# Optimization experiments

Measured on AMD Instinct MI355X. Metric: run time of the kernel, lower is better.

Reference implementation:

```python
import jax, jax.numpy as jnp
import numpy as np

DIM = 1024
DEPTH = 2
HEADS = 16
MLP = 4096
HEAD_DIM = DIM // HEADS
EPS = 1e-5


def layernorm(x, w, b):
    mu = jnp.mean(x, axis=-1, keepdims=True)
    var = jnp.mean(jnp.square(x - mu), axis=-1, keepdims=True)
    return (x - mu) * jax.lax.rsqrt(var + EPS) * w + b


def setup_inputs() -> dict:
    key = jax.random.key(0)
    ks = jax.random.split(key, 16)
    s = 0.02
    x = jax.random.normal(ks[0], (2, 2048, DIM), dtype=jnp.float32)
    inp = {
        "x": x,
        "ln1_w": jnp.ones((DEPTH, DIM), jnp.float32),
        "ln1_b": jnp.zeros((DEPTH, DIM), jnp.float32),
        "qkv_w": jax.random.normal(ks[1], (DEPTH, DIM, 3 * DIM), jnp.float32) * s,
        "qkv_b": jnp.zeros((DEPTH, 3 * DIM), jnp.float32),
        "in_w": jax.random.normal(ks[2], (DEPTH, DIM, 3 * DIM), jnp.float32) * s,
        "in_b": jnp.zeros((DEPTH, 3 * DIM), jnp.float32),
        "out_w": jax.random.normal(ks[3], (DEPTH, DIM, DIM), jnp.float32) * s,
        "out_b": jnp.zeros((DEPTH, DIM), jnp.float32),
        "ln2_w": jnp.ones((DEPTH, DIM), jnp.float32),
        "ln2_b": jnp.zeros((DEPTH, DIM), jnp.float32),
        "w1": jax.random.normal(ks[4], (DEPTH, DIM, MLP), jnp.float32) * s,
        "b1": jnp.zeros((DEPTH, MLP), jnp.float32),
        "w2": jax.random.normal(ks[5], (DEPTH, MLP, DIM), jnp.float32) * s,
        "b2": jnp.zeros((DEPTH, DIM), jnp.float32),
    }
    return inp


def _forward(x, ln1_w, ln1_b, qkv_w, qkv_b, in_w, in_b, out_w, out_b,
             ln2_w, ln2_b, w1, b1, w2, b2):
    B, S, D = x.shape
    scale = 1.0 / jnp.sqrt(jnp.float32(HEAD_DIM))
    for i in range(DEPTH):
        # --- Attention block (pre-norm) ---
        h = layernorm(x, ln1_w[i], ln1_b[i])
        qkv = h @ qkv_w[i] + qkv_b[i]                      # [B,S,3D]
        q, k, v = jnp.split(qkv, 3, axis=-1)
        # nn.MultiheadAttention's own in_proj on top of to_qkv
        qp = q @ in_w[i][:, :D] + in_b[i][:D]
        kp = k @ in_w[i][:, D:2 * D] + in_b[i][D:2 * D]
        vp = v @ in_w[i][:, 2 * D:] + in_b[i][2 * D:]
        qp = qp.reshape(B, S, HEADS, HEAD_DIM)
        kp = kp.reshape(B, S, HEADS, HEAD_DIM)
        vp = vp.reshape(B, S, HEADS, HEAD_DIM)
        scores = jnp.einsum("bqhd,bkhd->bhqk", qp, kp) * scale
        attn = jax.nn.softmax(scores, axis=-1)
        o = jnp.einsum("bhqk,bkhd->bqhd", attn, vp).reshape(B, S, D)
        o = o @ out_w[i] + out_b[i]
        x = o + x
        # --- FFN block (pre-norm) ---
        h = layernorm(x, ln2_w[i], ln2_b[i])
        h = jax.nn.gelu(h @ w1[i] + b1[i], approximate=False)
        h = h @ w2[i] + b2[i]
        x = h + x
    return x


def reference(x, ln1_w, ln1_b, qkv_w, qkv_b, in_w, in_b, out_w, out_b,
              ln2_w, ln2_b, w1, b1, w2, b2):
    return _forward(x, ln1_w, ln1_b, qkv_w, qkv_b, in_w, in_b, out_w, out_b,
                    ln2_w, ln2_b, w1, b1, w2, b2)
```

## Files before the change

kernel.cpp:

```cpp
#include <hip/hip_runtime.h>
#include <math.h>

#define D_MODEL 1024
#define NHEADS 16
#define HEAD_DIM 64
#define SEQ 2048
#define BATCH 2
#define TOK (BATCH*SEQ)
#define MLP_DIM 4096

#define F_BIAS  1
#define F_GELU  2

typedef __attribute__((ext_vector_type(8))) __bf16 bf16x8;
typedef __attribute__((ext_vector_type(16))) __bf16 bf16x16;
typedef __attribute__((ext_vector_type(4))) __bf16 bf16x4;
typedef __attribute__((ext_vector_type(4))) float f32x4;

__device__ __forceinline__ void gload16(const void* g, void* l) {
    __builtin_amdgcn_global_load_lds(
        (const __attribute__((address_space(1))) void*)g,
        (__attribute__((address_space(3))) void*)l, 16, 0, 0);
}

__global__ __launch_bounds__(256)
void conv_kernel(const float* __restrict__ in, __bf16* __restrict__ out, int n8)
{
    const int idx = blockIdx.x * 256 + threadIdx.x;
    if (idx >= n8) return;
    const float4 a = *(const float4*)(in + idx * 8);
    const float4 b = *(const float4*)(in + idx * 8 + 4);
    bf16x8 o;
    o[0] = (__bf16)a.x; o[1] = (__bf16)a.y; o[2] = (__bf16)a.z; o[3] = (__bf16)a.w;
    o[4] = (__bf16)b.x; o[5] = (__bf16)b.y; o[6] = (__bf16)b.z; o[7] = (__bf16)b.w;
    *(bf16x8*)(out + idx * 8) = o;
}

__global__ __launch_bounds__(256)
void tconv64_kernel(const float* __restrict__ in, __bf16* __restrict__ out, int R, int C)
{
    __shared__ __bf16 tile[64][72];
    const int bx = blockIdx.x;
    const int by = blockIdx.y;
    const int t = threadIdx.x;
    const int rl = t >> 4, cl = (t & 15) * 4;
    #pragma unroll
    for (int rr = 0; rr < 4; ++rr) {
        const float4 v = *(const float4*)&in[(size_t)(by * 64 + rr * 16 + rl) * C + bx * 64 + cl];
        tile[rr * 16 + rl][cl + 0] = (__bf16)v.x;
        tile[rr * 16 + rl][cl + 1] = (__bf16)v.y;
        tile[rr * 16 + rl][cl + 2] = (__bf16)v.z;
        tile[rr * 16 + rl][cl + 3] = (__bf16)v.w;
    }
    __syncthreads();
    const int oc = t >> 2, rs = (t & 3) * 16;
    bf16x16 y;
    #pragma unroll
    for (int k = 0; k < 16; ++k) y[k] = tile[rs + k][oc];
    *(bf16x16*)&out[(size_t)(bx * 64 + oc) * R + by * 64 + rs] = y;
}

__global__ __launch_bounds__(256)
void bcomb_kernel(const float* __restrict__ qkv_b, const float* __restrict__ in_w,
                  const float* __restrict__ in_b, float* __restrict__ bc)
{
    const int t = blockIdx.x * 256 + threadIdx.x;
    const int p = t >> 10, n = t & 1023;
    float s = in_b[t];
    #pragma unroll 16
    for (int k = 0; k < D_MODEL; ++k)
        s = fmaf(qkv_b[p * D_MODEL + k], in_w[(size_t)k * 3 * D_MODEL + p * D_MODEL + n], s);
    bc[t] = s;
}

__global__ __launch_bounds__(256)
void tv_kernel(const __bf16* __restrict__ v, __bf16* __restrict__ vt)
{
    __shared__ __bf16 t[64][72];
    const int bh = blockIdx.y, b = bh >> 4, h = bh & 15;
    const int s0 = blockIdx.x * 64;
    const int r = threadIdx.x >> 3;
    const int c = (threadIdx.x & 7) * 8;
    #pragma unroll
    for (int rr = 0; rr < 64; rr += 32) {
        bf16x8 x = *(const bf16x8*)&v[(size_t)(b * SEQ + s0 + r + rr) * D_MODEL + h * 64 + c];
        #pragma unroll
        for (int k = 0; k < 8; ++k) t[r + rr][c + k] = x[k];
    }
    __syncthreads();
    #pragma unroll
    for (int rr = 0; rr < 64; rr += 32) {
        bf16x8 y;
        #pragma unroll
        for (int k = 0; k < 8; ++k) y[k] = t[c + k][r + rr];
        *(bf16x8*)&vt[((size_t)bh * 64 + r + rr) * SEQ + s0 + c] = y;
    }
}

__device__ __forceinline__ void ln_body(float4 v, const float* w, const float* b,
                                        __bf16* out, int row, int t)
{
    float s  = v.x + v.y + v.z + v.w;
    float ss = v.x*v.x + v.y*v.y + v.z*v.z + v.w*v.w;
    #pragma unroll
    for (int off = 32; off > 0; off >>= 1) {
        s  += __shfl_down(s, off);
        ss += __shfl_down(ss, off);
    }
    __shared__ float red[8];
    const int wid = t >> 6, lane = t & 63;
    if (lane == 0) { red[wid] = s; red[4 + wid] = ss; }
    __syncthreads();
    const float st  = red[0] + red[1] + red[2] + red[3];
    const float sst = red[4] + red[5] + red[6] + red[7];
    const float mu  = st * (1.0f / D_MODEL);
    const float var = sst * (1.0f / D_MODEL) - mu * mu;
    const float rs  = rsqrtf(var + 1e-5f);
    const float4 wv = *(const float4*)(w + t * 4);
    const float4 bv = *(const float4*)(b + t * 4);
    bf16x4 o;
    o[0] = (__bf16)((v.x - mu) * rs * wv.x + bv.x);
    o[1] = (__bf16)((v.y - mu) * rs * wv.y + bv.y);
    o[2] = (__bf16)((v.z - mu) * rs * wv.z + bv.z);
    o[3] = (__bf16)((v.w - mu) * rs * wv.w + bv.w);
    *(bf16x4*)(out + (size_t)row * D_MODEL + t * 4) = o;
}

__global__ __launch_bounds__(256)
void ln_kernel(const float* __restrict__ x, const float* __restrict__ w,
               const float* __restrict__ b, __bf16* __restrict__ out)
{
    const int row = blockIdx.x, t = threadIdx.x;
    float4 v = *(const float4*)(x + (size_t)row * D_MODEL + t * 4);
    ln_body(v, w, b, out, row, t);
}

__global__ __launch_bounds__(256)
void ln_add_kernel(float* __restrict__ x, const float* __restrict__ p0,
                   const float* __restrict__ p1, const float* __restrict__ w,
                   const float* __restrict__ b, __bf16* __restrict__ out)
{
    const int row = blockIdx.x, t = threadIdx.x;
    const size_t idx = (size_t)row * D_MODEL + t * 4;
    float4 v  = *(const float4*)(x + idx);
    float4 a0 = *(const float4*)(p0 + idx);
    float4 a1 = *(const float4*)(p1 + idx);
    v.x += a0.x + a1.x; v.y += a0.y + a1.y;
    v.z += a0.z + a1.z; v.w += a0.w + a1.w;
    *(float4*)(x + idx) = v;
    ln_body(v, w, b, out, row, t);
}

__global__ __launch_bounds__(256)
void add2_kernel(float* __restrict__ x, const float* __restrict__ p0,
                 const float* __restrict__ p1)
{
    const size_t idx = ((size_t)blockIdx.x * 256 + threadIdx.x) * 4;
    float4 v  = *(const float4*)(x + idx);
    float4 a0 = *(const float4*)(p0 + idx);
    float4 a1 = *(const float4*)(p1 + idx);
    v.x += a0.x + a1.x; v.y += a0.y + a1.y;
    v.z += a0.z + a1.z; v.w += a0.w + a1.w;
    *(float4*)(x + idx) = v;
}

__device__ __forceinline__ void mgemm_acc(
    const __bf16* __restrict__ A, int lda,
    const __bf16* __restrict__ Bt, int ldb, int K,
    __bf16* As, __bf16* Bs, f32x4 (&acc)[4][4])
{
    const int tid  = threadIdx.x;
    const int lane = tid & 63;
    const int w    = tid >> 6;
    const int wm   = w >> 1, wn = w & 1;
    const int bm = blockIdx.y, bn = blockIdx.x;

    const int s1 = 256 + tid;
    const int kc0 = tid >> 7, r0 = tid & 127;
    const int kc1 = s1  >> 7, r1 = s1 & 127;

    const __bf16* a0p = A  + (size_t)(bm * 128 + r0) * lda + kc0 * 8;
    const __bf16* a1p = A  + (size_t)(bm * 128 + r1) * lda + kc1 * 8;
    const __bf16* b0p = Bt + (size_t)(bn * 128 + r0) * ldb + kc0 * 8;
    const __bf16* b1p = Bt + (size_t)(bn * 128 + r1) * ldb + kc1 * 8;

    const int sl0 = (0 * 256 + w * 64) * 8;
    const int sl1 = (1 * 256 + w * 64) * 8;

    const int kq = lane >> 4;
    const int fr = lane & 15;
    const int aidx = (kq * 128 + wm * 64 + fr) * 8;
    const int bidx = (kq * 128 + wn * 64 + fr) * 8;

    auto STG = [&](int buf, int k0) {
        gload16(a0p + k0, As + buf * 4096 + sl0);
        gload16(a1p + k0, As + buf * 4096 + sl1);
        gload16(b0p + k0, Bs + buf * 4096 + sl0);
        gload16(b1p + k0, Bs + buf * 4096 + sl1);
    };

    STG(0, 0);
    __syncthreads();
    int cur = 0;
    for (int k0 = 0; k0 < K; k0 += 32) {
        if (k0 + 32 < K) STG(cur ^ 1, k0 + 32);
        const __bf16* as = As + cur * 4096;
        const __bf16* bs = Bs + cur * 4096;
        bf16x8 af[4], bfr[4];
        #pragma unroll
        for (int i = 0; i < 4; ++i) {
            af[i]  = *(const bf16x8*)&as[aidx + i * 128];
            bfr[i] = *(const bf16x8*)&bs[bidx + i * 128];
        }
        #pragma unroll
        for (int i = 0; i < 4; ++i)
            #pragma unroll
            for (int j = 0; j < 4; ++j)
                acc[i][j] = __builtin_amdgcn_mfma_f32_16x16x32_bf16(
                    af[i], bfr[j], acc[i][j], 0, 0, 0);
        __syncthreads();
        cur ^= 1;
    }
}

template<int FLAGS, typename CT>
__global__ __launch_bounds__(256)
void mgemm_z(const __bf16* __restrict__ A, int lda, long long sAz,
             const __bf16* __restrict__ Bt, int ldb, long long sBz,
             const float* __restrict__ bias, long long sbz,
             CT* __restrict__ C, int ldc, long long sCz, int K)
{
    __shared__ __bf16 As[2 * 4096];
    __shared__ __bf16 Bs[2 * 4096];
    const int z = blockIdx.z;
    A  += (size_t)z * sAz;
    Bt += (size_t)z * sBz;
    C  += (size_t)z * sCz;
    if (FLAGS & F_BIAS) bias += (size_t)z * sbz;

    f32x4 acc[4][4];
    #pragma unroll
    for (int i = 0; i < 4; ++i)
        #pragma unroll
        for (int j = 0; j < 4; ++j)
            acc[i][j] = (f32x4){0.f, 0.f, 0.f, 0.f};

    mgemm_acc(A, lda, Bt, ldb, K, As, Bs, acc);

    const int lane = threadIdx.x & 63;
    const int w    = threadIdx.x >> 6;
    const int row0 = blockIdx.y * 128 + (w >> 1) * 64 + (lane >> 4) * 4;
    const int col0 = blockIdx.x * 128 + (w & 1) * 64 + (lane & 15);
    #pragma unroll
    for (int i = 0; i < 4; ++i) {
        #pragma unroll
        for (int j = 0; j < 4; ++j) {
            const int col = col0 + j * 16;
            float bb = (FLAGS & F_BIAS) ? bias[col] : 0.0f;
            #pragma unroll
            for (int e = 0; e < 4; ++e) {
                const int row = row0 + i * 16 + e;
                C[(size_t)row * ldc + col] = (CT)(acc[i][j][e] + bb);
            }
        }
    }
}

template<int BN, int WM, int FLAGS, bool PROJ3, bool SPLITK>
__global__ __launch_bounds__(512)
void gs_kernel(const __bf16* __restrict__ A, int lda,
               const __bf16* __restrict__ Bt, int ldb,
               const float* __restrict__ bias,
               void* __restrict__ Cv, int ldc, int K, long long sCz)
{
    constexpr int WN = 8 / WM, RW = 256 / WM, CW = BN / WN;
    constexpr int MI = RW / 16, NJ = CW / 16;
    constexpr int LA = 4, LB = BN / 64;
    __shared__ __align__(16) __bf16 As[2][256 * 64];
    __shared__ __align__(16) __bf16 Bs[2][BN * 64];

    const int gx = gridDim.x;
    const int nwg = gx * gridDim.y;
    int lin = blockIdx.y * gx + blockIdx.x;
    lin = (lin & 7) * (nwg >> 3) + (lin >> 3);
    const int bm = lin / gx, bn = lin % gx;

    const int z = SPLITK ? blockIdx.z : 0;
    const __bf16* Ab = A  + (size_t)bm * 256 * lda + (size_t)z * K;
    const __bf16* Bb = Bt + (size_t)bn * BN  * ldb + (size_t)z * K;

    const int tid = threadIdx.x, lane = tid & 63, w = tid >> 6;
    const int wm = w / WN, wn = w % WN;
    const int kq = lane >> 4, fr = lane & 15;
    const int l8 = lane >> 3;
    const int swz = (lane & 7) ^ l8;

    const __bf16* aPtr[LA]; int aLds[LA];
    #pragma unroll
    for (int c = 0; c < LA; ++c) {
        aPtr[c] = Ab + (size_t)(c * 64 + w * 8 + l8) * lda + swz * 8;
        aLds[c] = (c * 512 + w * 64) * 8;
    }
    const __bf16* bPtr[LB]; int bLds[LB];
    #pragma unroll
    for (int c = 0; c < LB; ++c) {
        bPtr[c] = Bb + (size_t)(c * 64 + w * 8 + l8) * ldb + swz * 8;
        bLds[c] = (c * 512 + w * 64) * 8;
    }

    f32x4 acc[MI][NJ];
    #pragma unroll
    for (int i = 0; i < MI; ++i)
        #pragma unroll
        for (int j = 0; j < NJ; ++j)
            acc[i][j] = (f32x4){0.f, 0.f, 0.f, 0.f};

    auto STG = [&](int buf, int k0) {
        #pragma unroll
        for (int c = 0; c < LA; ++c)
            gload16(aPtr[c] + k0, &As[buf][aLds[c]]);
        #pragma unroll
        for (int c = 0; c < LB; ++c)
            gload16(bPtr[c] + k0, &Bs[buf][bLds[c]]);
    };

    const int fsw = fr & 7;
    auto COMPUTE = [&](int buf) {
        #pragma unroll
        for (int kk = 0; kk < 2; ++kk) {
            const int kc = (kk * 4 + kq) ^ fsw;
            bf16x8 af[MI], bfr[NJ];
            #pragma unroll
            for (int i = 0; i < MI; ++i)
                af[i] = *(const bf16x8*)&As[buf][(wm * RW + i * 16 + fr) * 64 + kc * 8];
            #pragma unroll
            for (int j = 0; j < NJ; ++j)
                bfr[j] = *(const bf16x8*)&Bs[buf][(wn * CW + j * 16 + fr) * 64 + kc * 8];
            #pragma unroll
            for (int i = 0; i < MI; ++i)
                #pragma unroll
                for (int j = 0; j < NJ; ++j)
                    acc[i][j] = __builtin_amdgcn_mfma_f32_16x16x32_bf16(
                        af[i], bfr[j], acc[i][j], 0, 0, 0);
        }
    };

    const int T = K >> 6;
    STG(0, 0);
    __syncthreads();
    int cur = 0;
    for (int t = 0; t < T; ++t) {
        if (t + 1 < T) STG(cur ^ 1, (t + 1) * 64);
        COMPUTE(cur);
        __syncthreads();
        cur ^= 1;
    }

    const int row0 = bm * 256 + wm * RW + kq * 4;
    const int col0 = bn * BN + wn * CW + fr;
    if (SPLITK) {
        float* P = (float*)Cv + (size_t)z * sCz;
        #pragma unroll
        for (int i = 0; i < MI; ++i) {
            #pragma unroll
            for (int j = 0; j < NJ; ++j) {
                const int col = col0 + j * 16;
                const float bb = (z == 0) ? bias[col] : 0.0f;
                #pragma unroll
                for (int e = 0; e < 4; ++e)
                    P[(size_t)(row0 + i * 16 + e) * ldc + col] = acc[i][j][e] + bb;
            }
        }
    } else {
        __bf16* C = (__bf16*)Cv;
        #pragma unroll
        for (int i = 0; i < MI; ++i) {
            #pragma unroll
            for (int j = 0; j < NJ; ++j) {
                const int col = col0 + j * 16;
                const float bb = (FLAGS & F_BIAS) ? bias[col] : 0.0f;
                #pragma unroll
                for (int e = 0; e < 4; ++e) {
                    const int row = row0 + i * 16 + e;
                    float val = acc[i][j][e] + bb;
                    if (FLAGS & F_GELU)
                        val = 0.5f * val * (1.0f + erff(val * 0.70710678118654752f));
                    if (PROJ3)
                        C[(size_t)(col >> 10) * TOK * D_MODEL +
                          (size_t)row * D_MODEL + (col & 1023)] = (__bf16)val;
                    else
                        C[(size_t)row * ldc + col] = (__bf16)val;
                }
            }
        }
    }
}

__global__ __launch_bounds__(256)
void attn4_kernel(const __bf16* __restrict__ qp, const __bf16* __restrict__ kp,
                  const __bf16* __restrict__ vt, __bf16* __restrict__ o)
{
    const int bh = blockIdx.y;
    const int b = bh >> 4, h = bh & 15;
    const int tid = threadIdx.x;
    const int lane = tid & 63;
    const int w = tid >> 6;
    const int g = lane >> 4;
    const int fr = lane & 15;
    const int q0 = blockIdx.x * 64 + w * 16;
    const int l8 = lane >> 3, swz = (lane & 7) ^ l8, fsw = fr & 7;

    __shared__ __align__(16) __bf16 Ks[2][64 * 64];
    __shared__ __align__(16) __bf16 Vs[2][64 * 64];
    __shared__ __align__(16) __bf16 Ps[4][16 * 72];

    const __bf16* qb = qp + (size_t)(b * SEQ + q0 + fr) * D_MODEL + h * HEAD_DIM;
    const bf16x8 qf0 = *(const bf16x8*)(qb + g * 8);
    const bf16x8 qf1 = *(const bf16x8*)(qb + 32 + g * 8);

    const __bf16* kb = kp + (size_t)(b * SEQ) * D_MODEL + h * HEAD_DIM;
    const __bf16* vb = vt + (size_t)bh * HEAD_DIM * SEQ;

    const __bf16* kPtr[2]; const __bf16* vPtr[2]; int sLds[2];
    #pragma unroll
    for (int c = 0; c < 2; ++c) {
        const int row = c * 32 + w * 8 + l8;
        kPtr[c] = kb + (size_t)row * D_MODEL + swz * 8;
        vPtr[c] = vb + (size_t)row * SEQ + swz * 8;
        sLds[c] = (c * 256 + w * 64) * 8;
    }

    auto STG = [&](int buf, int kv0) {
        #pragma unroll
        for (int c = 0; c < 2; ++c)
            gload16(kPtr[c] + (size_t)kv0 * D_MODEL, &Ks[buf][sLds[c]]);
        #pragma unroll
        for (int c = 0; c < 2; ++c)
            gload16(vPtr[c] + kv0, &Vs[buf][sLds[c]]);
    };

    f32x4 acc_o[4];
    #pragma unroll
    for (int dj = 0; dj < 4; ++dj) acc_o[dj] = (f32x4){0.f, 0.f, 0.f, 0.f};
    float m_run = -1e30f, l_run = 0.0f;

    STG(0, 0);
    __syncthreads();
    int tb = 0;
    for (int kv0 = 0; kv0 < SEQ; kv0 += 64) {
        if (kv0 + 64 < SEQ) STG(tb ^ 1, kv0 + 64);

        f32x4 sacc[4];
        __builtin_amdgcn_s_setprio(1);
        #pragma unroll
        for (int t = 0; t < 4; ++t) {
            const bf16x8 kf0 = *(const bf16x8*)&Ks[tb][(t * 16 + fr) * 64 + ((g    ) ^ fsw) * 8];
            const bf16x8 kf1 = *(const bf16x8*)&Ks[tb][(t * 16 + fr) * 64 + ((4 + g) ^ fsw) * 8];
            sacc[t] = __builtin_amdgcn_mfma_f32_16x16x32_bf16(
                kf0, qf0, (f32x4){0.f, 0.f, 0.f, 0.f}, 0, 0, 0);
            sacc[t] = __builtin_amdgcn_mfma_f32_16x16x32_bf16(kf1, qf1, sacc[t], 0, 0, 0);
        }
        __builtin_amdgcn_s_setprio(0);

        float mx = -1e30f;
        #pragma unroll
        for (int t = 0; t < 4; ++t)
            #pragma unroll
            for (int e = 0; e < 4; ++e) mx = fmaxf(mx, sacc[t][e]);
        mx *= 0.125f;
        mx = fmaxf(mx, __shfl_xor(mx, 16));
        mx = fmaxf(mx, __shfl_xor(mx, 32));
        const float m_new = fmaxf(m_run, mx);
        const float corr = __expf(m_run - m_new);
        float lsum = 0.0f;
        #pragma unroll
        for (int t = 0; t < 4; ++t) {
            bf16x4 pv;
            #pragma unroll
            for (int e = 0; e < 4; ++e) {
                const float p = __expf(sacc[t][e] * 0.125f - m_new);
                lsum += p;
                pv[e] = (__bf16)p;
            }
            *(bf16x4*)&Ps[w][fr * 72 + t * 16 + g * 4] = pv;
        }
        lsum += __shfl_xor(lsum, 16);
        lsum += __shfl_xor(lsum, 32);
        l_run = l_run * corr + lsum;
        m_run = m_new;
        #pragma unroll
        for (int dj = 0; dj < 4; ++dj)
            #pragma unroll
            for (int e = 0; e < 4; ++e) acc_o[dj][e] *= corr;

        __builtin_amdgcn_s_setprio(1);
        #pragma unroll
        for (int c = 0; c < 2; ++c) {
            const bf16x8 pf = *(const bf16x8*)&Ps[w][fr * 72 + c * 32 + g * 8];
            #pragma unroll
            for (int dj = 0; dj < 4; ++dj) {
                const bf16x8 vf = *(const bf16x8*)&Vs[tb][(dj * 16 + fr) * 64 +
                                                         ((c * 4 + g) ^ fsw) * 8];
                acc_o[dj] = __builtin_amdgcn_mfma_f32_16x16x32_bf16(vf, pf, acc_o[dj], 0, 0, 0);
            }
        }
        __builtin_amdgcn_s_setprio(0);
        __syncthreads();
        tb ^= 1;
    }

    const float inv = 1.0f / l_run;
    __bf16* orow = o + (size_t)(b * SEQ + q0 + fr) * D_MODEL + h * HEAD_DIM;
    #pragma unroll
    for (int dj = 0; dj < 4; ++dj) {
        bf16x4 t;
        #pragma unroll
        for (int e = 0; e < 4; ++e) t[e] = (__bf16)(acc_o[dj][e] * inv);
        *(bf16x4*)&orow[dj * 16 + g * 4] = t;
    }
}

extern "C" void kernel_launch(void* const* d_in, const int* in_sizes, int n_in,
                              void* d_out, int out_size, void* d_ws, size_t ws_size,
                              hipStream_t stream)
{
    const float* x    = (const float*)d_in[0];
    const float* ln1w = (const float*)d_in[1];
    const float* ln1b = (const float*)d_in[2];
    const float* qkvw = (const float*)d_in[3];
    const float* qkvb = (const float*)d_in[4];
    const float* inw  = (const float*)d_in[5];
    const float* inb  = (const float*)d_in[6];
    const float* outw = (const float*)d_in[7];
    const float* outb = (const float*)d_in[8];
    const float* ln2w = (const float*)d_in[9];
    const float* ln2b = (const float*)d_in[10];
    const float* w1   = (const float*)d_in[11];
    const float* b1   = (const float*)d_in[12];
    const float* w2   = (const float*)d_in[13];
    const float* b2   = (const float*)d_in[14];
    float* xo = (float*)d_out;

    const size_t OFF_WCT = 0;
    const size_t OFF_OUT = 3145728;
    const size_t OFF_W1  = 4194304;
    const size_t OFF_W2  = 8388608;
    const size_t L_WT    = 12582912;

    __bf16* WT   = (__bf16*)d_ws;
    __bf16* QKVb = WT + 2 * L_WT;
    __bf16* INt  = QKVb + 3145728;
    __bf16* X8   = INt + 3145728;
    __bf16* U_   = X8 + 4194304;
    __bf16* QKV3 = U_ + 16777216;
    __bf16* VT   = QKV3 + 12582912;
    float*  BC   = (float*)(VT + 4194304);
    float*  P_   = (float*)QKV3;

    hipMemcpyAsync(xo, x, (size_t)TOK * D_MODEL * sizeof(float),
                   hipMemcpyDeviceToDevice, stream);

    const dim3 blk(256);
    for (int i = 0; i < 2; ++i) {
        __bf16* wl = WT + i * L_WT;
        const float* l_qkvw = qkvw + (size_t)i * D_MODEL * 3 * D_MODEL;
        const float* l_inw  = inw  + (size_t)i * D_MODEL * 3 * D_MODEL;
        conv_kernel<<<1536, blk, 0, stream>>>(l_qkvw, QKVb, 393216);
        tconv64_kernel<<<dim3(48, 16), blk, 0, stream>>>(l_inw, INt, D_MODEL, 3 * D_MODEL);
        mgemm_z<0, __bf16><<<dim3(8, 8, 3), blk, 0, stream>>>(
            INt, D_MODEL, 1048576, QKVb, 3 * D_MODEL, D_MODEL,
            nullptr, 0, wl + OFF_WCT, D_MODEL, 1048576, D_MODEL);
        bcomb_kernel<<<12, blk, 0, stream>>>(
            qkvb + (size_t)i * 3 * D_MODEL, l_inw, inb + (size_t)i * 3 * D_MODEL,
            BC + (size_t)i * 3 * D_MODEL);
        tconv64_kernel<<<dim3(16, 16), blk, 0, stream>>>(
            outw + (size_t)i * D_MODEL * D_MODEL, wl + OFF_OUT, D_MODEL, D_MODEL);
        tconv64_kernel<<<dim3(64, 16), blk, 0, stream>>>(
            w1 + (size_t)i * D_MODEL * MLP_DIM, wl + OFF_W1, D_MODEL, MLP_DIM);
        tconv64_kernel<<<dim3(16, 64), blk, 0, stream>>>(
            w2 + (size_t)i * MLP_DIM * D_MODEL, wl + OFF_W2, MLP_DIM, D_MODEL);
    }

    for (int i = 0; i < 2; ++i) {
        __bf16* wl = WT + i * L_WT;
        const float* l_outb = outb + (size_t)i * D_MODEL;
        const float* l_b1   = b1   + (size_t)i * MLP_DIM;
        const float* l_b2   = b2   + (size_t)i * D_MODEL;

        if (i == 0)
            ln_kernel<<<TOK, blk, 0, stream>>>(xo, ln1w, ln1b, X8);
        gs_kernel<256, 2, F_BIAS, true, false><<<dim3(12, 16), 512, 0, stream>>>(
            X8, D_MODEL, wl + OFF_WCT, D_MODEL,
            BC + (size_t)i * 3 * D_MODEL, QKV3, D_MODEL, D_MODEL, 0);
        tv_kernel<<<dim3(SEQ / 64, BATCH * NHEADS), blk, 0, stream>>>(
            QKV3 + (size_t)2 * TOK * D_MODEL, VT);
        attn4_kernel<<<dim3(SEQ / 64, BATCH * NHEADS), blk, 0, stream>>>(
            QKV3, QKV3 + (size_t)TOK * D_MODEL, VT, X8);
        gs_kernel<128, 4, F_BIAS, false, true><<<dim3(8, 16, 2), 512, 0, stream>>>(
            X8, D_MODEL, wl + OFF_OUT, D_MODEL, l_outb, P_, D_MODEL, 512,
            (long long)TOK * D_MODEL);
        ln_add_kernel<<<TOK, blk, 0, stream>>>(
            xo, P_, P_ + (size_t)TOK * D_MODEL,
            ln2w + (size_t)i * D_MODEL, ln2b + (size_t)i * D_MODEL, X8);
        gs_kernel<256, 2, F_BIAS | F_GELU, false, false><<<dim3(16, 16), 512, 0, stream>>>(
            X8, D_MODEL, wl + OFF_W1, D_MODEL, l_b1, U_, MLP_DIM, D_MODEL, 0);
        gs_kernel<128, 4, F_BIAS, false, true><<<dim3(8, 16, 2), 512, 0, stream>>>(
            U_, MLP_DIM, wl + OFF_W2, MLP_DIM, l_b2, P_, D_MODEL, 2048,
            (long long)TOK * D_MODEL);
        if (i == 0) {
            ln_add_kernel<<<TOK, blk, 0, stream>>>(
                xo, P_, P_ + (size_t)TOK * D_MODEL,
                ln1w + D_MODEL, ln1b + D_MODEL, X8);
        } else {
            add2_kernel<<<TOK * D_MODEL / 1024, blk, 0, stream>>>(
                xo, P_, P_ + (size_t)TOK * D_MODEL);
        }
    }
}
```

Before: 747.0 us.

## Fold softmax scale into Q projection, lazy rescale, MFMA row sums

The Q projection epilogue now multiplies Q by scale*log2(e), so attention can use exp2 directly without a per-element scale. The online softmax skips rescaling the accumulators unless the running max grows by more than 8 (in log2 units), and the row sum is computed with an extra MFMA against a ones vector instead of shuffles. The weight-combine GEMM now reuses the main gs_kernel, launched three times, in place of the separate mgemm kernel. Risks are bf16 rounding of the pre-scaled Q and larger exponent values when rescaling is deferred.

```diff
diff --git a/kernel.cpp b/kernel.cpp
--- a/kernel.cpp
+++ b/kernel.cpp
@@ -11,6 +11,7 @@
 
 #define F_BIAS  1
 #define F_GELU  2
+#define QSCALE 0.18033688011112042f
 
 typedef __attribute__((ext_vector_type(8))) __bf16 bf16x8;
 typedef __attribute__((ext_vector_type(16))) __bf16 bf16x16;
@@ -164,108 +165,6 @@
     *(float4*)(x + idx) = v;
 }
 
-__device__ __forceinline__ void mgemm_acc(
-    const __bf16* __restrict__ A, int lda,
-    const __bf16* __restrict__ Bt, int ldb, int K,
-    __bf16* As, __bf16* Bs, f32x4 (&acc)[4][4])
-{
-    const int tid  = threadIdx.x;
-    const int lane = tid & 63;
-    const int w    = tid >> 6;
-    const int wm   = w >> 1, wn = w & 1;
-    const int bm = blockIdx.y, bn = blockIdx.x;
-
-    const int s1 = 256 + tid;
-    const int kc0 = tid >> 7, r0 = tid & 127;
-    const int kc1 = s1  >> 7, r1 = s1 & 127;
-
-    const __bf16* a0p = A  + (size_t)(bm * 128 + r0) * lda + kc0 * 8;
-    const __bf16* a1p = A  + (size_t)(bm * 128 + r1) * lda + kc1 * 8;
-    const __bf16* b0p = Bt + (size_t)(bn * 128 + r0) * ldb + kc0 * 8;
-    const __bf16* b1p = Bt + (size_t)(bn * 128 + r1) * ldb + kc1 * 8;
-
-    const int sl0 = (0 * 256 + w * 64) * 8;
-    const int sl1 = (1 * 256 + w * 64) * 8;
-
-    const int kq = lane >> 4;
-    const int fr = lane & 15;
-    const int aidx = (kq * 128 + wm * 64 + fr) * 8;
-    const int bidx = (kq * 128 + wn * 64 + fr) * 8;
-
-    auto STG = [&](int buf, int k0) {
-        gload16(a0p + k0, As + buf * 4096 + sl0);
-        gload16(a1p + k0, As + buf * 4096 + sl1);
-        gload16(b0p + k0, Bs + buf * 4096 + sl0);
-        gload16(b1p + k0, Bs + buf * 4096 + sl1);
-    };
-
-    STG(0, 0);
-    __syncthreads();
-    int cur = 0;
-    for (int k0 = 0; k0 < K; k0 += 32) {
-        if (k0 + 32 < K) STG(cur ^ 1, k0 + 32);
-        const __bf16* as = As + cur * 4096;
-        const __bf16* bs = Bs + cur * 4096;
-        bf16x8 af[4], bfr[4];
-        #pragma unroll
-        for (int i = 0; i < 4; ++i) {
-            af[i]  = *(const bf16x8*)&as[aidx + i * 128];
-            bfr[i] = *(const bf16x8*)&bs[bidx + i * 128];
-        }
-        #pragma unroll
-        for (int i = 0; i < 4; ++i)
-            #pragma unroll
-            for (int j = 0; j < 4; ++j)
-                acc[i][j] = __builtin_amdgcn_mfma_f32_16x16x32_bf16(
-                    af[i], bfr[j], acc[i][j], 0, 0, 0);
-        __syncthreads();
-        cur ^= 1;
-    }
-}
-
-template<int FLAGS, typename CT>
-__global__ __launch_bounds__(256)
-void mgemm_z(const __bf16* __restrict__ A, int lda, long long sAz,
-             const __bf16* __restrict__ Bt, int ldb, long long sBz,
-             const float* __restrict__ bias, long long sbz,
-             CT* __restrict__ C, int ldc, long long sCz, int K)
-{
-    __shared__ __bf16 As[2 * 4096];
-    __shared__ __bf16 Bs[2 * 4096];
-    const int z = blockIdx.z;
-    A  += (size_t)z * sAz;
-    Bt += (size_t)z * sBz;
-    C  += (size_t)z * sCz;
-    if (FLAGS & F_BIAS) bias += (size_t)z * sbz;
-
-    f32x4 acc[4][4];
-    #pragma unroll
-    for (int i = 0; i < 4; ++i)
-        #pragma unroll
-        for (int j = 0; j < 4; ++j)
-            acc[i][j] = (f32x4){0.f, 0.f, 0.f, 0.f};
-
-    mgemm_acc(A, lda, Bt, ldb, K, As, Bs, acc);
-
-    const int lane = threadIdx.x & 63;
-    const int w    = threadIdx.x >> 6;
-    const int row0 = blockIdx.y * 128 + (w >> 1) * 64 + (lane >> 4) * 4;
-    const int col0 = blockIdx.x * 128 + (w & 1) * 64 + (lane & 15);
-    #pragma unroll
-    for (int i = 0; i < 4; ++i) {
-        #pragma unroll
-        for (int j = 0; j < 4; ++j) {
-            const int col = col0 + j * 16;
-            float bb = (FLAGS & F_BIAS) ? bias[col] : 0.0f;
-            #pragma unroll
-            for (int e = 0; e < 4; ++e) {
-                const int row = row0 + i * 16 + e;
-                C[(size_t)row * ldc + col] = (CT)(acc[i][j][e] + bb);
-            }
-        }
-    }
-}
-
 template<int BN, int WM, int FLAGS, bool PROJ3, bool SPLITK>
 __global__ __launch_bounds__(512)
 void gs_kernel(const __bf16* __restrict__ A, int lda,
@@ -385,11 +284,13 @@
                     float val = acc[i][j][e] + bb;
                     if (FLAGS & F_GELU)
                         val = 0.5f * val * (1.0f + erff(val * 0.70710678118654752f));
-                    if (PROJ3)
+                    if (PROJ3) {
+                        if ((col >> 10) == 0) val *= QSCALE;
                         C[(size_t)(col >> 10) * TOK * D_MODEL +
                           (size_t)row * D_MODEL + (col & 1023)] = (__bf16)val;
-                    else
+                    } else {
                         C[(size_t)row * ldc + col] = (__bf16)val;
+                    }
                 }
             }
         }
@@ -397,7 +298,7 @@
 }
 
 __global__ __launch_bounds__(256)
-void attn4_kernel(const __bf16* __restrict__ qp, const __bf16* __restrict__ kp,
+void attn5_kernel(const __bf16* __restrict__ qp, const __bf16* __restrict__ kp,
                   const __bf16* __restrict__ vt, __bf16* __restrict__ o)
 {
     const int bh = blockIdx.y;
@@ -439,10 +340,15 @@
             gload16(vPtr[c] + kv0, &Vs[buf][sLds[c]]);
     };
 
+    bf16x8 vone;
+    #pragma unroll
+    for (int k = 0; k < 8; ++k) vone[k] = (__bf16)1.0f;
+
     f32x4 acc_o[4];
     #pragma unroll
     for (int dj = 0; dj < 4; ++dj) acc_o[dj] = (f32x4){0.f, 0.f, 0.f, 0.f};
-    float m_run = -1e30f, l_run = 0.0f;
+    f32x4 acc_l = (f32x4){0.f, 0.f, 0.f, 0.f};
+    float m_run = -1e30f;
 
     STG(0, 0);
     __syncthreads();
@@ -462,41 +368,40 @@
         }
         __builtin_amdgcn_s_setprio(0);
 
-        float mx = -1e30f;
-        #pragma unroll
-        for (int t = 0; t < 4; ++t)
-            #pragma unroll
-            for (int e = 0; e < 4; ++e) mx = fmaxf(mx, sacc[t][e]);
-        mx *= 0.125f;
+        float m0 = fmaxf(fmaxf(sacc[0][0], sacc[0][1]), fmaxf(sacc[0][2], sacc[0][3]));
+        float m1 = fmaxf(fmaxf(sacc[1][0], sacc[1][1]), fmaxf(sacc[1][2], sacc[1][3]));
+        float m2 = fmaxf(fmaxf(sacc[2][0], sacc[2][1]), fmaxf(sacc[2][2], sacc[2][3]));
+        float m3 = fmaxf(fmaxf(sacc[3][0], sacc[3][1]), fmaxf(sacc[3][2], sacc[3][3]));
+        float mx = fmaxf(fmaxf(m0, m1), fmaxf(m2, m3));
         mx = fmaxf(mx, __shfl_xor(mx, 16));
         mx = fmaxf(mx, __shfl_xor(mx, 32));
-        const float m_new = fmaxf(m_run, mx);
-        const float corr = __expf(m_run - m_new);
-        float lsum = 0.0f;
+
+        if (!__all(mx <= m_run + 8.0f)) {
+            const float m_new = fmaxf(m_run, mx);
+            const float corr = exp2f(m_run - m_new);
+            m_run = m_new;
+            #pragma unroll
+            for (int dj = 0; dj < 4; ++dj)
+                #pragma unroll
+                for (int e = 0; e < 4; ++e) acc_o[dj][e] *= corr;
+            #pragma unroll
+            for (int e = 0; e < 4; ++e) acc_l[e] *= corr;
+        }
+
         #pragma unroll
         for (int t = 0; t < 4; ++t) {
             bf16x4 pv;
             #pragma unroll
-            for (int e = 0; e < 4; ++e) {
-                const float p = __expf(sacc[t][e] * 0.125f - m_new);
-                lsum += p;
-                pv[e] = (__bf16)p;
-            }
+            for (int e = 0; e < 4; ++e)
+                pv[e] = (__bf16)exp2f(sacc[t][e] - m_run);
             *(bf16x4*)&Ps[w][fr * 72 + t * 16 + g * 4] = pv;
         }
-        lsum += __shfl_xor(lsum, 16);
-        lsum += __shfl_xor(lsum, 32);
-        l_run = l_run * corr + lsum;
-        m_run = m_new;
-        #pragma unroll
-        for (int dj = 0; dj < 4; ++dj)
-            #pragma unroll
-            for (int e = 0; e < 4; ++e) acc_o[dj][e] *= corr;
 
         __builtin_amdgcn_s_setprio(1);
         #pragma unroll
         for (int c = 0; c < 2; ++c) {
             const bf16x8 pf = *(const bf16x8*)&Ps[w][fr * 72 + c * 32 + g * 8];
+            acc_l = __builtin_amdgcn_mfma_f32_16x16x32_bf16(vone, pf, acc_l, 0, 0, 0);
             #pragma unroll
             for (int dj = 0; dj < 4; ++dj) {
                 const bf16x8 vf = *(const bf16x8*)&Vs[tb][(dj * 16 + fr) * 64 +
@@ -509,7 +414,7 @@
         tb ^= 1;
     }
 
-    const float inv = 1.0f / l_run;
+    const float inv = 1.0f / acc_l[0];
     __bf16* orow = o + (size_t)(b * SEQ + q0 + fr) * D_MODEL + h * HEAD_DIM;
     #pragma unroll
     for (int dj = 0; dj < 4; ++dj) {
@@ -567,9 +472,12 @@
         const float* l_inw  = inw  + (size_t)i * D_MODEL * 3 * D_MODEL;
         conv_kernel<<<1536, blk, 0, stream>>>(l_qkvw, QKVb, 393216);
         tconv64_kernel<<<dim3(48, 16), blk, 0, stream>>>(l_inw, INt, D_MODEL, 3 * D_MODEL);
-        mgemm_z<0, __bf16><<<dim3(8, 8, 3), blk, 0, stream>>>(
-            INt, D_MODEL, 1048576, QKVb, 3 * D_MODEL, D_MODEL,
-            nullptr, 0, wl + OFF_WCT, D_MODEL, 1048576, D_MODEL);
+        for (int p = 0; p < 3; ++p) {
+            gs_kernel<256, 2, 0, false, false><<<dim3(4, 4), 512, 0, stream>>>(
+                INt + (size_t)p * 1048576, D_MODEL,
+                QKVb + (size_t)p * D_MODEL, 3 * D_MODEL,
+                nullptr, wl + OFF_WCT + (size_t)p * 1048576, D_MODEL, D_MODEL, 0);
+        }
         bcomb_kernel<<<12, blk, 0, stream>>>(
             qkvb + (size_t)i * 3 * D_MODEL, l_inw, inb + (size_t)i * 3 * D_MODEL,
             BC + (size_t)i * 3 * D_MODEL);
@@ -594,7 +502,7 @@
             BC + (size_t)i * 3 * D_MODEL, QKV3, D_MODEL, D_MODEL, 0);
         tv_kernel<<<dim3(SEQ / 64, BATCH * NHEADS), blk, 0, stream>>>(
             QKV3 + (size_t)2 * TOK * D_MODEL, VT);
-        attn4_kernel<<<dim3(SEQ / 64, BATCH * NHEADS), blk, 0, stream>>>(
+        attn5_kernel<<<dim3(SEQ / 64, BATCH * NHEADS), blk, 0, stream>>>(
             QKV3, QKV3 + (size_t)TOK * D_MODEL, VT, X8);
         gs_kernel<128, 4, F_BIAS, false, true><<<dim3(8, 16, 2), 512, 0, stream>>>(
             X8, D_MODEL, wl + OFF_OUT, D_MODEL, l_outb, P_, D_MODEL, 512,
```

New measurement: 894.0 us. 1.2x slower.
